# Optimization experiments

Measured on AMD Instinct MI355X. Metric: run time of the kernel, lower is better.

The kernel has to match this reference:

```python
import jax, jax.numpy as jnp
import numpy as np

B, L, D = 16384, 50, 32  # batch, history length, embedding_dim
NU, NI, NC = 100000, 100000, 1000


def setup_inputs() -> dict:
    key = jax.random.key(0)
    ks = jax.random.split(key, 16)
    customer_id = jax.random.randint(ks[0], (B,), 0, NU)
    candidate_good = jax.random.randint(ks[1], (B,), 0, NI)
    candidate_class = jax.random.randint(ks[2], (B,), 0, NC)
    history_goods = jax.random.randint(ks[3], (B, L), 0, NI)
    history_classes = jax.random.randint(ks[4], (B, L), 0, NC)
    user_table = jax.random.normal(ks[5], (NU, D), jnp.float32) * 0.05
    item_table = jax.random.normal(ks[6], (NI, D), jnp.float32) * 0.05
    item_table = item_table.at[0].set(0.0)  # padding_idx=0
    cat_table = jax.random.normal(ks[7], (NC, D), jnp.float32) * 0.05
    cat_table = cat_table.at[0].set(0.0)  # padding_idx=0
    # attention net: Linear(4*2D=256 -> 80), Linear(80 -> 1)
    aw1 = jax.random.normal(ks[8], (4 * 2 * D, 80), jnp.float32) * 0.05
    ab1 = jnp.zeros((80,), jnp.float32)
    aw2 = jax.random.normal(ks[9], (80, 1), jnp.float32) * 0.05
    ab2 = jnp.zeros((1,), jnp.float32)
    # final mlp: 5D=160 -> 256 -> 128 -> 1
    mw1 = jax.random.normal(ks[10], (5 * D, 256), jnp.float32) * 0.05
    mb1 = jnp.zeros((256,), jnp.float32)
    mw2 = jax.random.normal(ks[11], (256, 128), jnp.float32) * 0.05
    mb2 = jnp.zeros((128,), jnp.float32)
    mw3 = jax.random.normal(ks[12], (128, 1), jnp.float32) * 0.05
    mb3 = jnp.zeros((1,), jnp.float32)
    return dict(customer_id=customer_id, candidate_good=candidate_good,
                candidate_class=candidate_class, history_goods=history_goods,
                history_classes=history_classes, user_table=user_table,
                item_table=item_table, cat_table=cat_table,
                aw1=aw1, ab1=ab1, aw2=aw2, ab2=ab2,
                mw1=mw1, mb1=mb1, mw2=mw2, mb2=mb2, mw3=mw3, mb3=mb3)


def reference(customer_id, candidate_good, candidate_class, history_goods,
              history_classes, user_table, item_table, cat_table,
              aw1, ab1, aw2, ab2, mw1, mb1, mw2, mb2, mw3, mb3):
    user_emb = user_table[customer_id]                               # [B, D]
    cand = jnp.concatenate([item_table[candidate_good],
                            cat_table[candidate_class]], axis=-1)    # [B, 2D]
    hist = jnp.concatenate([item_table[history_goods],
                            cat_table[history_classes]], axis=-1)    # [B, L, 2D]
    q = jnp.broadcast_to(cand[:, None, :], hist.shape)               # [B, L, 2D]
    info = jnp.concatenate([q, hist, q - hist, q * hist], axis=-1)   # [B, L, 8D]
    h = jax.nn.relu(info @ aw1 + ab1)                                # [B, L, 80]
    scores = (h @ aw2 + ab2)[..., 0]                                 # [B, L]
    mask = history_goods != 0
    scores = jnp.where(mask, scores, -1e9)
    weights = jax.nn.softmax(scores, axis=1)                         # [B, L]
    att = jnp.einsum('bl,bld->bd', weights, hist)                    # [B, 2D]
    combined = jnp.concatenate([user_emb, cand, att], axis=-1)       # [B, 5D]
    z = jax.nn.relu(combined @ mw1 + mb1)
    z = jax.nn.relu(z @ mw2 + mb2)
    out = (z @ mw3 + mb3)[..., 0]                                    # [B]
    return out
```

## Files before the change

kernel.cpp:

```cpp
#include <hip/hip_runtime.h>
#include <math.h>

#define LHIST 50

typedef __attribute__((ext_vector_type(8))) short bf16x8;
typedef __attribute__((ext_vector_type(4))) float f32x4;

__device__ __forceinline__ unsigned short f2bf(float f) {
    union { float f; unsigned u; } v; v.f = f;
    unsigned r = v.u + 0x7fff + ((v.u >> 16) & 1);
    return (unsigned short)(r >> 16);
}
__device__ __forceinline__ float bf2f(unsigned short h) {
    union { unsigned u; float f; } v; v.u = ((unsigned)h) << 16;
    return v.f;
}
__device__ __forceinline__ unsigned packbf2(float lo, float hi) {
    return (unsigned)f2bf(lo) | ((unsigned)f2bf(hi) << 16);
}


__global__ void prep_kernel(const float* __restrict__ aw1,
                            const float* __restrict__ mw1,
                            const float* __restrict__ mw2,
                            const float* __restrict__ item_table,
                            const float* __restrict__ cat_table,
                            int itemN, int catN,
                            float* __restrict__ Awt,
                            unsigned short* __restrict__ Bmfb,
                            unsigned short* __restrict__ W4fb,
                            unsigned short* __restrict__ W1f,
                            unsigned short* __restrict__ W2f,
                            unsigned short* __restrict__ itemb,
                            unsigned short* __restrict__ catb) {
    int i = blockIdx.x * 256 + threadIdx.x;
    int i8 = i * 8;
    if (i8 + 7 < itemN) {
        float4 a = *(const float4*)&item_table[i8];
        float4 b = *(const float4*)&item_table[i8 + 4];
        uint4 r;
        r.x = packbf2(a.x, a.y); r.y = packbf2(a.z, a.w);
        r.z = packbf2(b.x, b.y); r.w = packbf2(b.z, b.w);
        *(uint4*)&itemb[i8] = r;
    }
    if (i8 + 7 < catN) {
        float4 a = *(const float4*)&cat_table[i8];
        float4 b = *(const float4*)&cat_table[i8 + 4];
        uint4 r;
        r.x = packbf2(a.x, a.y); r.y = packbf2(a.z, a.w);
        r.z = packbf2(b.x, b.y); r.w = packbf2(b.z, b.w);
        *(uint4*)&catb[i8] = r;
    }
    if (i < 5120) {
        int j = i >> 6, k = i & 63;
        Awt[i] = aw1[k * 80 + j] + aw1[(128 + k) * 80 + j];
        int kk = i / 80, n = i - kk * 80;
        int nt = n >> 4, colw = n & 15, ks = kk >> 5, r = kk & 31, qd = r >> 3, off = r & 7;
        int d = ((nt * 2 + ks) * 64 + qd * 16 + colw) * 8 + off;
        Bmfb[d] = f2bf(aw1[(64 + kk) * 80 + n] - aw1[(128 + kk) * 80 + n]);
        W4fb[d] = f2bf(aw1[(192 + kk) * 80 + n]);
    }
    if (i < 40960) {
        int kk = i >> 8, n = i & 255;
        int nt = n >> 4, colw = n & 15, ks = kk >> 5, r = kk & 31, qd = r >> 3, off = r & 7;
        W1f[((nt * 5 + ks) * 64 + qd * 16 + colw) * 8 + off] = f2bf(mw1[i]);
    }
    if (i < 32768) {
        int kk = i >> 7, n = i & 127;
        int nt = n >> 4, colw = n & 15, ks = kk >> 5, r = kk & 31, qd = r >> 3, off = r & 7;
        W2f[((nt * 8 + ks) * 64 + qd * 16 + colw) * 8 + off] = f2bf(mw2[i]);
    }
}

__global__ void __launch_bounds__(256, 4) attn_kernel(
    const int* __restrict__ cid, const int* __restrict__ cg,
    const int* __restrict__ cc,  const int* __restrict__ hg,
    const int* __restrict__ hc,
    const float* __restrict__ user_table, const float* __restrict__ item_table,
    const float* __restrict__ cat_table,
    const float* __restrict__ ab1, const float* __restrict__ aw2,
    const float* __restrict__ Awt, const unsigned short* __restrict__ Bmfb,
    const unsigned short* __restrict__ W4fb,
    const unsigned short* __restrict__ itemb, const unsigned short* __restrict__ catb,
    unsigned short* __restrict__ cfrag)
{
    __shared__ __align__(16) unsigned short sh_Bq[4][5120];
    __shared__ __align__(16) float sh_q[4][64];
    __shared__ float sh_bias[4][80];
    __shared__ float sh_sc[4][64];
    __shared__ float sh_aw2[80];
    __shared__ __align__(16) float sh_att[4][64];

    const int t = threadIdx.x;
    const int b0 = blockIdx.x * 4;
    const int wv = t >> 6;
    const int lane = t & 63;
    const int quad = lane >> 4;
    const int col = lane & 15;
    const int b = b0 + wv;

    int il[4], ic[4];
    #pragma unroll
    for (int mt = 0; mt < 4; ++mt) {
        int l = mt * 16 + col;
        int lc = (l < LHIST) ? l : 0;
        il[mt] = hg[b * LHIST + lc];
        ic[mt] = hc[b * LHIST + lc];
    }
    uint4 vi[4], vc[4];
    #pragma unroll
    for (int mt = 0; mt < 4; ++mt) {
        vi[mt] = *(const uint4*)&itemb[(size_t)il[mt] * 32 + quad * 8];
        vc[mt] = *(const uint4*)&catb[(size_t)ic[mt] * 32 + quad * 8];
    }
    {
        float v = (lane < 32) ? item_table[(size_t)cg[b] * 32 + lane]
                              : cat_table[(size_t)cc[b] * 32 + (lane - 32)];
        sh_q[wv][lane] = v;
    }
    if (t < 80) sh_aw2[t] = aw2[t];
    __syncthreads();

    #pragma unroll
    for (int it = 0; it < 10; ++it) {
        int i = it * 256 + t;
        int bb = i / 640;
        int j = (i - bb * 640) * 8;
        int lane8 = (j >> 3) & 63, ks = (j >> 9) & 1;
        int kk = ks * 32 + (lane8 >> 4) * 8;
        uint4 bm4 = *(const uint4*)&Bmfb[j];
        uint4 w44 = *(const uint4*)&W4fb[j];
        float4 qa = *(const float4*)&sh_q[bb][kk];
        float4 qb = *(const float4*)&sh_q[bb][kk + 4];
        unsigned bmw[4] = {bm4.x, bm4.y, bm4.z, bm4.w};
        unsigned w4w[4] = {w44.x, w44.y, w44.z, w44.w};
        float qv[8] = {qa.x, qa.y, qa.z, qa.w, qb.x, qb.y, qb.z, qb.w};
        uint4 res;
        unsigned* rp = (unsigned*)&res;
        #pragma unroll
        for (int d = 0; d < 4; ++d) {
            float lo = bf2f((unsigned short)(bmw[d] & 0xffff)) + qv[2 * d]     * bf2f((unsigned short)(w4w[d] & 0xffff));
            float hi = bf2f((unsigned short)(bmw[d] >> 16))    + qv[2 * d + 1] * bf2f((unsigned short)(w4w[d] >> 16));
            rp[d] = packbf2(lo, hi);
        }
        *(uint4*)&sh_Bq[bb][j] = res;
    }
    for (int s = t; s < 320; s += 256) {
        int bi = s / 80, j = s - bi * 80;
        float acc = ab1[j];
        const float4* aw = (const float4*)&Awt[j * 64];
        #pragma unroll
        for (int k4 = 0; k4 < 16; ++k4) {
            float4 a = aw[k4];
            float4 q = *(const float4*)&sh_q[bi][k4 * 4];
            acc += a.x * q.x + a.y * q.y + a.z * q.z + a.w * q.w;
        }
        sh_bias[bi][j] = acc;
    }
    __syncthreads();

    float bias_v[5], a2_v[5];
    #pragma unroll
    for (int nt = 0; nt < 5; ++nt) {
        bias_v[nt] = sh_bias[wv][nt * 16 + col];
        a2_v[nt]   = sh_aw2[nt * 16 + col];
    }

    #pragma unroll
    for (int p = 0; p < 2; ++p) {
        f32x4 acc[2][5];
        #pragma unroll
        for (int mi = 0; mi < 2; ++mi)
            #pragma unroll
            for (int nt = 0; nt < 5; ++nt) acc[mi][nt] = (f32x4){0.f,0.f,0.f,0.f};
        bf16x8 a0i = *(bf16x8*)&vi[p * 2];
        bf16x8 a0c = *(bf16x8*)&vc[p * 2];
        bf16x8 a1i = *(bf16x8*)&vi[p * 2 + 1];
        bf16x8 a1c = *(bf16x8*)&vc[p * 2 + 1];
        #pragma unroll
        for (int nt = 0; nt < 5; ++nt) {
            bf16x8 b0 = *(const bf16x8*)&sh_Bq[wv][((nt * 2 + 0) * 64 + lane) * 8];
            acc[0][nt] = __builtin_amdgcn_mfma_f32_16x16x32_bf16(a0i, b0, acc[0][nt], 0, 0, 0);
            acc[1][nt] = __builtin_amdgcn_mfma_f32_16x16x32_bf16(a1i, b0, acc[1][nt], 0, 0, 0);
            bf16x8 b1 = *(const bf16x8*)&sh_Bq[wv][((nt * 2 + 1) * 64 + lane) * 8];
            acc[0][nt] = __builtin_amdgcn_mfma_f32_16x16x32_bf16(a0c, b1, acc[0][nt], 0, 0, 0);
            acc[1][nt] = __builtin_amdgcn_mfma_f32_16x16x32_bf16(a1c, b1, acc[1][nt], 0, 0, 0);
        }
        #pragma unroll
        for (int mi = 0; mi < 2; ++mi) {
            int mt = p * 2 + mi;
            #pragma unroll
            for (int i = 0; i < 4; ++i) {
                float pp = 0.f;
                #pragma unroll
                for (int nt = 0; nt < 5; ++nt) {
                    float u = acc[mi][nt][i] + bias_v[nt];
                    pp += fmaxf(u, 0.f) * a2_v[nt];
                }
                pp += __shfl_xor(pp, 1);
                pp += __shfl_xor(pp, 2);
                pp += __shfl_xor(pp, 4);
                pp += __shfl_xor(pp, 8);
                if (col == 0) sh_sc[wv][mt * 16 + quad * 4 + i] = pp;
            }
        }
    }

    float sc = -INFINITY;
    if (lane < LHIST) {
        sc = sh_sc[wv][lane];
        if (hg[b * LHIST + lane] == 0) sc = -1e9f;
    }
    float m = sc;
    #pragma unroll
    for (int off = 32; off > 0; off >>= 1) m = fmaxf(m, __shfl_xor(m, off));
    float e = (lane < LHIST) ? __expf(sc - m) : 0.f;
    float ssum = e;
    #pragma unroll
    for (int off = 32; off > 0; off >>= 1) ssum += __shfl_xor(ssum, off);
    float w = e / ssum;

    {
        float wl[4];
        wl[0] = __shfl(w, col);
        wl[1] = __shfl(w, 16 + col);
        wl[2] = __shfl(w, 32 + col);
        wl[3] = __shfl(w, 48 + col);
        float at0[8], at1[8];
        #pragma unroll
        for (int j = 0; j < 8; ++j) { at0[j] = 0.f; at1[j] = 0.f; }
        #pragma unroll
        for (int mt = 0; mt < 4; ++mt) {
            union { uint4 u; unsigned short s[8]; } hi, hcv;
            hi.u = vi[mt]; hcv.u = vc[mt];
            #pragma unroll
            for (int j = 0; j < 8; ++j) {
                at0[j] += wl[mt] * bf2f(hi.s[j]);
                at1[j] += wl[mt] * bf2f(hcv.s[j]);
            }
        }
        #pragma unroll
        for (int off = 1; off < 16; off <<= 1)
            #pragma unroll
            for (int j = 0; j < 8; ++j) {
                at0[j] += __shfl_xor(at0[j], off);
                at1[j] += __shfl_xor(at1[j], off);
            }
        if (col == 0) {
            *(float4*)&sh_att[wv][quad * 8]     = make_float4(at0[0], at0[1], at0[2], at0[3]);
            *(float4*)&sh_att[wv][quad * 8 + 4] = make_float4(at0[4], at0[5], at0[6], at0[7]);
            *(float4*)&sh_att[wv][32 + quad * 8]     = make_float4(at1[0], at1[1], at1[2], at1[3]);
            *(float4*)&sh_att[wv][32 + quad * 8 + 4] = make_float4(at1[4], at1[5], at1[6], at1[7]);
        }
    }

    {
        int g = b >> 4, colm = b & 15;
        unsigned short* base = cfrag + (size_t)g * 2560;
        if (lane < 8) {
            float4 aa = *(const float4*)&sh_att[wv][lane * 8];
            float4 ab = *(const float4*)&sh_att[wv][lane * 8 + 4];
            int k0 = 96 + lane * 8;
            int ks = k0 >> 5, qd = (k0 >> 3) & 3;
            uint4 r;
            r.x = packbf2(aa.x, aa.y); r.y = packbf2(aa.z, aa.w);
            r.z = packbf2(ab.x, ab.y); r.w = packbf2(ab.z, ab.w);
            *(uint4*)(base + ((ks * 64) + qd * 16 + colm) * 8) = r;
        } else if (lane < 16) {
            int cq = lane - 8;
            int k0 = 32 + cq * 8;
            int ks = k0 >> 5, qd = (k0 >> 3) & 3;
            float4 qa = *(const float4*)&sh_q[wv][cq * 8];
            float4 qb = *(const float4*)&sh_q[wv][cq * 8 + 4];
            uint4 r;
            r.x = packbf2(qa.x, qa.y); r.y = packbf2(qa.z, qa.w);
            r.z = packbf2(qb.x, qb.y); r.w = packbf2(qb.z, qb.w);
            *(uint4*)(base + ((ks * 64) + qd * 16 + colm) * 8) = r;
        } else if (lane < 20) {
            int cu = lane - 16;
            int uidx = cid[b];
            float4 ua = *(const float4*)&user_table[(size_t)uidx * 32 + cu * 8];
            float4 ub = *(const float4*)&user_table[(size_t)uidx * 32 + cu * 8 + 4];
            uint4 r;
            r.x = packbf2(ua.x, ua.y); r.y = packbf2(ua.z, ua.w);
            r.z = packbf2(ub.x, ub.y); r.w = packbf2(ub.z, ub.w);
            *(uint4*)(base + (cu * 16 + colm) * 8) = r;
        }
    }
}

__global__ void __launch_bounds__(256, 4) mlp_kernel(
    const unsigned short* __restrict__ cfrag,
    const unsigned short* __restrict__ W1f, const unsigned short* __restrict__ W2f,
    const float* __restrict__ mb1, const float* __restrict__ mb2,
    const float* __restrict__ mw3, const float* __restrict__ mb3,
    float* __restrict__ out)
{
    __shared__ __align__(16) unsigned short shA2[4096];
    __shared__ float sh_part[4][16];

    const int t = threadIdx.x;
    const int g = blockIdx.x;
    const int wv = t >> 6;
    const int lane = t & 63;
    const int quad = lane >> 4;
    const int col = lane & 15;
    const unsigned short* abase = cfrag + (size_t)g * 2560;

    f32x4 acc1[4];
    #pragma unroll
    for (int j = 0; j < 4; ++j) acc1[j] = (f32x4){0.f, 0.f, 0.f, 0.f};
    #pragma unroll
    for (int ks = 0; ks < 5; ++ks) {
        bf16x8 a = *(const bf16x8*)&abase[(ks * 64 + lane) * 8];
        #pragma unroll
        for (int j = 0; j < 4; ++j) {
            bf16x8 bw = *(const bf16x8*)&W1f[(((wv * 4 + j) * 5 + ks) * 64 + lane) * 8];
            acc1[j] = __builtin_amdgcn_mfma_f32_16x16x32_bf16(a, bw, acc1[j], 0, 0, 0);
        }
    }
    #pragma unroll
    for (int j = 0; j < 4; ++j) {
        int n = (wv * 4 + j) * 16 + col;
        float bj = mb1[n];
        int ks2 = n >> 5, qd2 = (n >> 3) & 3, off2 = n & 7;
        #pragma unroll
        for (int i = 0; i < 4; ++i) {
            float z = fmaxf(acc1[j][i] + bj, 0.f);
            shA2[(ks2 * 64 + qd2 * 16 + quad * 4 + i) * 8 + off2] = f2bf(z);
        }
    }
    __syncthreads();

    f32x4 acc2[2];
    #pragma unroll
    for (int jj = 0; jj < 2; ++jj) acc2[jj] = (f32x4){0.f, 0.f, 0.f, 0.f};
    #pragma unroll
    for (int ks = 0; ks < 8; ++ks) {
        bf16x8 a = *(const bf16x8*)&shA2[(ks * 64 + lane) * 8];
        #pragma unroll
        for (int jj = 0; jj < 2; ++jj) {
            bf16x8 bw = *(const bf16x8*)&W2f[(((wv * 2 + jj) * 8 + ks) * 64 + lane) * 8];
            acc2[jj] = __builtin_amdgcn_mfma_f32_16x16x32_bf16(a, bw, acc2[jj], 0, 0, 0);
        }
    }
    #pragma unroll
    for (int i = 0; i < 4; ++i) {
        float p = 0.f;
        #pragma unroll
        for (int jj = 0; jj < 2; ++jj) {
            int n = (wv * 2 + jj) * 16 + col;
            float z = fmaxf(acc2[jj][i] + mb2[n], 0.f);
            p += z * mw3[n];
        }
        p += __shfl_xor(p, 1);
        p += __shfl_xor(p, 2);
        p += __shfl_xor(p, 4);
        p += __shfl_xor(p, 8);
        if (col == 0) sh_part[wv][quad * 4 + i] = p;
    }
    __syncthreads();
    if (t < 16)
        out[g * 16 + t] = sh_part[0][t] + sh_part[1][t] + sh_part[2][t] + sh_part[3][t] + mb3[0];
}

extern "C" void kernel_launch(void* const* d_in, const int* in_sizes, int n_in,
                              void* d_out, int out_size, void* d_ws, size_t ws_size,
                              hipStream_t stream) {
    const int*   cid = (const int*)d_in[0];
    const int*   cg  = (const int*)d_in[1];
    const int*   cc  = (const int*)d_in[2];
    const int*   hg  = (const int*)d_in[3];
    const int*   hc  = (const int*)d_in[4];
    const float* user_table = (const float*)d_in[5];
    const float* item_table = (const float*)d_in[6];
    const float* cat_table  = (const float*)d_in[7];
    const float* aw1 = (const float*)d_in[8];
    const float* ab1 = (const float*)d_in[9];
    const float* aw2 = (const float*)d_in[10];
    const float* mw1 = (const float*)d_in[12];
    const float* mb1 = (const float*)d_in[13];
    const float* mw2 = (const float*)d_in[14];
    const float* mb2 = (const float*)d_in[15];
    const float* mw3 = (const float*)d_in[16];
    const float* mb3 = (const float*)d_in[17];
    float* out = (float*)d_out;

    const int B = in_sizes[0];
    const int itemN = in_sizes[6];
    const int catN  = in_sizes[7];
    float* ws = (float*)d_ws;
    float* Awt = ws;
    unsigned short* Bmfb = (unsigned short*)(ws + 5120);
    unsigned short* W4fb = (unsigned short*)(ws + 7680);
    unsigned short* W1f  = (unsigned short*)(ws + 10240);
    unsigned short* W2f  = (unsigned short*)(ws + 30720);
    unsigned short* itemb = (unsigned short*)(ws + 47104);
    unsigned short* catb  = itemb + itemN;
    unsigned short* cfrag = (unsigned short*)(ws + 47104 + (itemN + catN + 1) / 2);

    int n8 = (itemN + 7) / 8;
    int prep_grid = (n8 + 255) / 256;
    if (prep_grid < 160) prep_grid = 160;
    prep_kernel<<<prep_grid, 256, 0, stream>>>(aw1, mw1, mw2, item_table, cat_table,
                                               itemN, catN, Awt, Bmfb, W4fb, W1f, W2f,
                                               itemb, catb);
    attn_kernel<<<B / 4, 256, 0, stream>>>(cid, cg, cc, hg, hc,
                                           user_table, item_table, cat_table,
                                           ab1, aw2, Awt, Bmfb, W4fb, itemb, catb, cfrag);
    mlp_kernel<<<B / 16, 256, 0, stream>>>(cfrag, W1f, W2f,
                                           mb1, mb2, mw3, mb3, out);
}
```

Measured before the change: 211.5 us.

## Split each attention row across two waves and shrink attn blocks to two rows

The attention kernel now handles two batch rows per 256-thread block, with two waves sharing each row's 50-step history (32 positions each). Partial attention sums from the two halves are combined through shared memory before writing the MLP input fragment. This halves per-block shared memory and per-wave registers, doubles the grid, and raises the launch-bounds occupancy target to improve latency hiding on the gather-heavy kernel. It adds extra block barriers and a cross-wave reduction. Separately, bf16 packing switches to the HIP intrinsic conversion.

```diff
diff --git a/kernel.cpp b/kernel.cpp
--- a/kernel.cpp
+++ b/kernel.cpp
@@ -1,4 +1,5 @@
 #include <hip/hip_runtime.h>
+#include <hip/hip_bf16.h>
 #include <math.h>
 
 #define LHIST 50
@@ -18,6 +19,12 @@
 __device__ __forceinline__ unsigned packbf2(float lo, float hi) {
     return (unsigned)f2bf(lo) | ((unsigned)f2bf(hi) << 16);
 }
+__device__ __forceinline__ unsigned pk2(float lo, float hi) {
+    __hip_bfloat162 h = __float22bfloat162_rn(make_float2(lo, hi));
+    return *(unsigned*)&h;
+}
+__device__ __forceinline__ float bflo(unsigned u){ union{unsigned v;float f;} x; x.v = u << 16; return x.f; }
+__device__ __forceinline__ float bfhi(unsigned u){ union{unsigned v;float f;} x; x.v = u & 0xffff0000u; return x.f; }
 
 
 __global__ void prep_kernel(const float* __restrict__ aw1,
@@ -39,16 +46,16 @@
         float4 a = *(const float4*)&item_table[i8];
         float4 b = *(const float4*)&item_table[i8 + 4];
         uint4 r;
-        r.x = packbf2(a.x, a.y); r.y = packbf2(a.z, a.w);
-        r.z = packbf2(b.x, b.y); r.w = packbf2(b.z, b.w);
+        r.x = pk2(a.x, a.y); r.y = pk2(a.z, a.w);
+        r.z = pk2(b.x, b.y); r.w = pk2(b.z, b.w);
         *(uint4*)&itemb[i8] = r;
     }
     if (i8 + 7 < catN) {
         float4 a = *(const float4*)&cat_table[i8];
         float4 b = *(const float4*)&cat_table[i8 + 4];
         uint4 r;
-        r.x = packbf2(a.x, a.y); r.y = packbf2(a.z, a.w);
-        r.z = packbf2(b.x, b.y); r.w = packbf2(b.z, b.w);
+        r.x = pk2(a.x, a.y); r.y = pk2(a.z, a.w);
+        r.z = pk2(b.x, b.y); r.w = pk2(b.z, b.w);
         *(uint4*)&catb[i8] = r;
     }
     if (i < 5120) {
@@ -72,7 +79,7 @@
     }
 }
 
-__global__ void __launch_bounds__(256, 4) attn_kernel(
+__global__ void __launch_bounds__(256, 6) attn_kernel(
     const int* __restrict__ cid, const int* __restrict__ cg,
     const int* __restrict__ cc,  const int* __restrict__ hg,
     const int* __restrict__ hc,
@@ -84,69 +91,78 @@
     const unsigned short* __restrict__ itemb, const unsigned short* __restrict__ catb,
     unsigned short* __restrict__ cfrag)
 {
-    __shared__ __align__(16) unsigned short sh_Bq[4][5120];
-    __shared__ __align__(16) float sh_q[4][64];
-    __shared__ float sh_bias[4][80];
-    __shared__ float sh_sc[4][64];
+    __shared__ __align__(16) unsigned short sh_Bq[2][5120];
+    __shared__ __align__(16) float sh_q[2][64];
+    __shared__ float sh_bias[2][80];
+    __shared__ float sh_sc[2][64];
     __shared__ float sh_aw2[80];
-    __shared__ __align__(16) float sh_att[4][64];
+    __shared__ __align__(16) float sh_att[2][2][64];
 
     const int t = threadIdx.x;
-    const int b0 = blockIdx.x * 4;
+    const int b0 = blockIdx.x * 2;
     const int wv = t >> 6;
     const int lane = t & 63;
     const int quad = lane >> 4;
     const int col = lane & 15;
-    const int b = b0 + wv;
-
-    int il[4], ic[4];
-    #pragma unroll
-    for (int mt = 0; mt < 4; ++mt) {
-        int l = mt * 16 + col;
+    const int bb = wv >> 1;
+    const int hwv = wv & 1;
+    const int b = b0 + bb;
+
+    int il[2], ic[2];
+    #pragma unroll
+    for (int mi = 0; mi < 2; ++mi) {
+        int l = hwv * 32 + mi * 16 + col;
         int lc = (l < LHIST) ? l : 0;
-        il[mt] = hg[b * LHIST + lc];
-        ic[mt] = hc[b * LHIST + lc];
-    }
-    uint4 vi[4], vc[4];
-    #pragma unroll
-    for (int mt = 0; mt < 4; ++mt) {
-        vi[mt] = *(const uint4*)&itemb[(size_t)il[mt] * 32 + quad * 8];
-        vc[mt] = *(const uint4*)&catb[(size_t)ic[mt] * 32 + quad * 8];
-    }
-    {
-        float v = (lane < 32) ? item_table[(size_t)cg[b] * 32 + lane]
-                              : cat_table[(size_t)cc[b] * 32 + (lane - 32)];
-        sh_q[wv][lane] = v;
+        il[mi] = hg[b * LHIST + lc];
+        ic[mi] = hc[b * LHIST + lc];
+    }
+    uint4 vi[2], vc[2];
+    #pragma unroll
+    for (int mi = 0; mi < 2; ++mi) {
+        vi[mi] = *(const uint4*)&itemb[(size_t)il[mi] * 32 + quad * 8];
+        vc[mi] = *(const uint4*)&catb[(size_t)ic[mi] * 32 + quad * 8];
+    }
+    if (t < 128) {
+        int qbi = t >> 6, k = t & 63;
+        int bq = b0 + qbi;
+        float v = (k < 32) ? item_table[(size_t)cg[bq] * 32 + k]
+                           : cat_table[(size_t)cc[bq] * 32 + (k - 32)];
+        sh_q[qbi][k] = v;
     }
     if (t < 80) sh_aw2[t] = aw2[t];
     __syncthreads();
 
-    #pragma unroll
-    for (int it = 0; it < 10; ++it) {
-        int i = it * 256 + t;
-        int bb = i / 640;
-        int j = (i - bb * 640) * 8;
-        int lane8 = (j >> 3) & 63, ks = (j >> 9) & 1;
+    for (int slot = t; slot < 640; slot += 256) {
+        int j = slot * 8;
+        int lane8 = slot & 63, ks = (slot >> 6) & 1;
         int kk = ks * 32 + (lane8 >> 4) * 8;
         uint4 bm4 = *(const uint4*)&Bmfb[j];
         uint4 w44 = *(const uint4*)&W4fb[j];
-        float4 qa = *(const float4*)&sh_q[bb][kk];
-        float4 qb = *(const float4*)&sh_q[bb][kk + 4];
-        unsigned bmw[4] = {bm4.x, bm4.y, bm4.z, bm4.w};
-        unsigned w4w[4] = {w44.x, w44.y, w44.z, w44.w};
-        float qv[8] = {qa.x, qa.y, qa.z, qa.w, qb.x, qb.y, qb.z, qb.w};
-        uint4 res;
-        unsigned* rp = (unsigned*)&res;
+        unsigned bw[4] = {bm4.x, bm4.y, bm4.z, bm4.w};
+        unsigned ww[4] = {w44.x, w44.y, w44.z, w44.w};
+        float bl[8], wl4[8];
         #pragma unroll
         for (int d = 0; d < 4; ++d) {
-            float lo = bf2f((unsigned short)(bmw[d] & 0xffff)) + qv[2 * d]     * bf2f((unsigned short)(w4w[d] & 0xffff));
-            float hi = bf2f((unsigned short)(bmw[d] >> 16))    + qv[2 * d + 1] * bf2f((unsigned short)(w4w[d] >> 16));
-            rp[d] = packbf2(lo, hi);
-        }
-        *(uint4*)&sh_Bq[bb][j] = res;
-    }
-    for (int s = t; s < 320; s += 256) {
-        int bi = s / 80, j = s - bi * 80;
+            bl[2 * d] = bflo(bw[d]);  bl[2 * d + 1] = bfhi(bw[d]);
+            wl4[2 * d] = bflo(ww[d]); wl4[2 * d + 1] = bfhi(ww[d]);
+        }
+        #pragma unroll
+        for (int bb2 = 0; bb2 < 2; ++bb2) {
+            float4 qa = *(const float4*)&sh_q[bb2][kk];
+            float4 qb = *(const float4*)&sh_q[bb2][kk + 4];
+            float qv[8] = {qa.x, qa.y, qa.z, qa.w, qb.x, qb.y, qb.z, qb.w};
+            uint4 res;
+            unsigned* rp = (unsigned*)&res;
+            #pragma unroll
+            for (int d = 0; d < 4; ++d)
+                rp[d] = pk2(bl[2 * d]     + qv[2 * d]     * wl4[2 * d],
+                            bl[2 * d + 1] + qv[2 * d + 1] * wl4[2 * d + 1]);
+            *(uint4*)&sh_Bq[bb2][j] = res;
+        }
+    }
+    if (t < 160) {
+        int bi = t >= 80;
+        int j = t - bi * 80;
         float acc = ab1[j];
         const float4* aw = (const float4*)&Awt[j * 64];
         #pragma unroll
@@ -162,53 +178,50 @@
     float bias_v[5], a2_v[5];
     #pragma unroll
     for (int nt = 0; nt < 5; ++nt) {
-        bias_v[nt] = sh_bias[wv][nt * 16 + col];
+        bias_v[nt] = sh_bias[bb][nt * 16 + col];
         a2_v[nt]   = sh_aw2[nt * 16 + col];
     }
-
-    #pragma unroll
-    for (int p = 0; p < 2; ++p) {
-        f32x4 acc[2][5];
-        #pragma unroll
-        for (int mi = 0; mi < 2; ++mi)
+    f32x4 acc[2][5];
+    #pragma unroll
+    for (int mi = 0; mi < 2; ++mi)
+        #pragma unroll
+        for (int nt = 0; nt < 5; ++nt) acc[mi][nt] = (f32x4){0.f, 0.f, 0.f, 0.f};
+    bf16x8 a0i = *(bf16x8*)&vi[0];
+    bf16x8 a0c = *(bf16x8*)&vc[0];
+    bf16x8 a1i = *(bf16x8*)&vi[1];
+    bf16x8 a1c = *(bf16x8*)&vc[1];
+    #pragma unroll
+    for (int nt = 0; nt < 5; ++nt) {
+        bf16x8 bfr0 = *(const bf16x8*)&sh_Bq[bb][((nt * 2 + 0) * 64 + lane) * 8];
+        acc[0][nt] = __builtin_amdgcn_mfma_f32_16x16x32_bf16(a0i, bfr0, acc[0][nt], 0, 0, 0);
+        acc[1][nt] = __builtin_amdgcn_mfma_f32_16x16x32_bf16(a1i, bfr0, acc[1][nt], 0, 0, 0);
+        bf16x8 bfr1 = *(const bf16x8*)&sh_Bq[bb][((nt * 2 + 1) * 64 + lane) * 8];
+        acc[0][nt] = __builtin_amdgcn_mfma_f32_16x16x32_bf16(a0c, bfr1, acc[0][nt], 0, 0, 0);
+        acc[1][nt] = __builtin_amdgcn_mfma_f32_16x16x32_bf16(a1c, bfr1, acc[1][nt], 0, 0, 0);
+    }
+    #pragma unroll
+    for (int mi = 0; mi < 2; ++mi) {
+        int lbase = hwv * 32 + mi * 16 + quad * 4;
+        #pragma unroll
+        for (int i = 0; i < 4; ++i) {
+            float pp = 0.f;
             #pragma unroll
-            for (int nt = 0; nt < 5; ++nt) acc[mi][nt] = (f32x4){0.f,0.f,0.f,0.f};
-        bf16x8 a0i = *(bf16x8*)&vi[p * 2];
-        bf16x8 a0c = *(bf16x8*)&vc[p * 2];
-        bf16x8 a1i = *(bf16x8*)&vi[p * 2 + 1];
-        bf16x8 a1c = *(bf16x8*)&vc[p * 2 + 1];
-        #pragma unroll
-        for (int nt = 0; nt < 5; ++nt) {
-            bf16x8 b0 = *(const bf16x8*)&sh_Bq[wv][((nt * 2 + 0) * 64 + lane) * 8];
-            acc[0][nt] = __builtin_amdgcn_mfma_f32_16x16x32_bf16(a0i, b0, acc[0][nt], 0, 0, 0);
-            acc[1][nt] = __builtin_amdgcn_mfma_f32_16x16x32_bf16(a1i, b0, acc[1][nt], 0, 0, 0);
-            bf16x8 b1 = *(const bf16x8*)&sh_Bq[wv][((nt * 2 + 1) * 64 + lane) * 8];
-            acc[0][nt] = __builtin_amdgcn_mfma_f32_16x16x32_bf16(a0c, b1, acc[0][nt], 0, 0, 0);
-            acc[1][nt] = __builtin_amdgcn_mfma_f32_16x16x32_bf16(a1c, b1, acc[1][nt], 0, 0, 0);
-        }
-        #pragma unroll
-        for (int mi = 0; mi < 2; ++mi) {
-            int mt = p * 2 + mi;
-            #pragma unroll
-            for (int i = 0; i < 4; ++i) {
-                float pp = 0.f;
-                #pragma unroll
-                for (int nt = 0; nt < 5; ++nt) {
-                    float u = acc[mi][nt][i] + bias_v[nt];
-                    pp += fmaxf(u, 0.f) * a2_v[nt];
-                }
-                pp += __shfl_xor(pp, 1);
-                pp += __shfl_xor(pp, 2);
-                pp += __shfl_xor(pp, 4);
-                pp += __shfl_xor(pp, 8);
-                if (col == 0) sh_sc[wv][mt * 16 + quad * 4 + i] = pp;
+            for (int nt = 0; nt < 5; ++nt) {
+                float u = acc[mi][nt][i] + bias_v[nt];
+                pp += fmaxf(u, 0.f) * a2_v[nt];
             }
-        }
-    }
+            pp += __shfl_xor(pp, 1);
+            pp += __shfl_xor(pp, 2);
+            pp += __shfl_xor(pp, 4);
+            pp += __shfl_xor(pp, 8);
+            if (col == 0) sh_sc[bb][lbase + i] = pp;
+        }
+    }
+    __syncthreads();
 
     float sc = -INFINITY;
     if (lane < LHIST) {
-        sc = sh_sc[wv][lane];
+        sc = sh_sc[bb][lane];
         if (hg[b * LHIST + lane] == 0) sc = -1e9f;
     }
     float m = sc;
@@ -221,22 +234,20 @@
     float w = e / ssum;
 
     {
-        float wl[4];
-        wl[0] = __shfl(w, col);
-        wl[1] = __shfl(w, 16 + col);
-        wl[2] = __shfl(w, 32 + col);
-        wl[3] = __shfl(w, 48 + col);
+        float wl[2];
+        wl[0] = __shfl(w, hwv * 32 + col);
+        wl[1] = __shfl(w, hwv * 32 + 16 + col);
         float at0[8], at1[8];
         #pragma unroll
         for (int j = 0; j < 8; ++j) { at0[j] = 0.f; at1[j] = 0.f; }
         #pragma unroll
-        for (int mt = 0; mt < 4; ++mt) {
+        for (int mi = 0; mi < 2; ++mi) {
             union { uint4 u; unsigned short s[8]; } hi, hcv;
-            hi.u = vi[mt]; hcv.u = vc[mt];
+            hi.u = vi[mi]; hcv.u = vc[mi];
             #pragma unroll
             for (int j = 0; j < 8; ++j) {
-                at0[j] += wl[mt] * bf2f(hi.s[j]);
-                at1[j] += wl[mt] * bf2f(hcv.s[j]);
+                at0[j] += wl[mi] * bf2f(hi.s[j]);
+                at1[j] += wl[mi] * bf2f(hcv.s[j]);
             }
         }
         #pragma unroll
@@ -247,24 +258,28 @@
                 at1[j] += __shfl_xor(at1[j], off);
             }
         if (col == 0) {
-            *(float4*)&sh_att[wv][quad * 8]     = make_float4(at0[0], at0[1], at0[2], at0[3]);
-            *(float4*)&sh_att[wv][quad * 8 + 4] = make_float4(at0[4], at0[5], at0[6], at0[7]);
-            *(float4*)&sh_att[wv][32 + quad * 8]     = make_float4(at1[0], at1[1], at1[2], at1[3]);
-            *(float4*)&sh_att[wv][32 + quad * 8 + 4] = make_float4(at1[4], at1[5], at1[6], at1[7]);
-        }
-    }
-
-    {
-        int g = b >> 4, colm = b & 15;
+            *(float4*)&sh_att[bb][hwv][quad * 8]     = make_float4(at0[0], at0[1], at0[2], at0[3]);
+            *(float4*)&sh_att[bb][hwv][quad * 8 + 4] = make_float4(at0[4], at0[5], at0[6], at0[7]);
+            *(float4*)&sh_att[bb][hwv][32 + quad * 8]     = make_float4(at1[0], at1[1], at1[2], at1[3]);
+            *(float4*)&sh_att[bb][hwv][32 + quad * 8 + 4] = make_float4(at1[4], at1[5], at1[6], at1[7]);
+        }
+    }
+    __syncthreads();
+
+    if (wv < 2) {
+        int bo = b0 + wv;
+        int g = bo >> 4, colm = bo & 15;
         unsigned short* base = cfrag + (size_t)g * 2560;
         if (lane < 8) {
-            float4 aa = *(const float4*)&sh_att[wv][lane * 8];
-            float4 ab = *(const float4*)&sh_att[wv][lane * 8 + 4];
+            float4 a0 = *(const float4*)&sh_att[wv][0][lane * 8];
+            float4 a1 = *(const float4*)&sh_att[wv][1][lane * 8];
+            float4 b0v = *(const float4*)&sh_att[wv][0][lane * 8 + 4];
+            float4 b1v = *(const float4*)&sh_att[wv][1][lane * 8 + 4];
             int k0 = 96 + lane * 8;
             int ks = k0 >> 5, qd = (k0 >> 3) & 3;
             uint4 r;
-            r.x = packbf2(aa.x, aa.y); r.y = packbf2(aa.z, aa.w);
-            r.z = packbf2(ab.x, ab.y); r.w = packbf2(ab.z, ab.w);
+            r.x = pk2(a0.x + a1.x, a0.y + a1.y); r.y = pk2(a0.z + a1.z, a0.w + a1.w);
+            r.z = pk2(b0v.x + b1v.x, b0v.y + b1v.y); r.w = pk2(b0v.z + b1v.z, b0v.w + b1v.w);
             *(uint4*)(base + ((ks * 64) + qd * 16 + colm) * 8) = r;
         } else if (lane < 16) {
             int cq = lane - 8;
@@ -273,17 +288,17 @@
             float4 qa = *(const float4*)&sh_q[wv][cq * 8];
             float4 qb = *(const float4*)&sh_q[wv][cq * 8 + 4];
             uint4 r;
-            r.x = packbf2(qa.x, qa.y); r.y = packbf2(qa.z, qa.w);
-            r.z = packbf2(qb.x, qb.y); r.w = packbf2(qb.z, qb.w);
+            r.x = pk2(qa.x, qa.y); r.y = pk2(qa.z, qa.w);
+            r.z = pk2(qb.x, qb.y); r.w = pk2(qb.z, qb.w);
             *(uint4*)(base + ((ks * 64) + qd * 16 + colm) * 8) = r;
         } else if (lane < 20) {
             int cu = lane - 16;
-            int uidx = cid[b];
+            int uidx = cid[bo];
             float4 ua = *(const float4*)&user_table[(size_t)uidx * 32 + cu * 8];
             float4 ub = *(const float4*)&user_table[(size_t)uidx * 32 + cu * 8 + 4];
             uint4 r;
-            r.x = packbf2(ua.x, ua.y); r.y = packbf2(ua.z, ua.w);
-            r.z = packbf2(ub.x, ub.y); r.w = packbf2(ub.z, ub.w);
+            r.x = pk2(ua.x, ua.y); r.y = pk2(ua.z, ua.w);
+            r.z = pk2(ub.x, ub.y); r.w = pk2(ub.z, ub.w);
             *(uint4*)(base + (cu * 16 + colm) * 8) = r;
         }
     }
@@ -405,7 +420,7 @@
     prep_kernel<<<prep_grid, 256, 0, stream>>>(aw1, mw1, mw2, item_table, cat_table,
                                                itemN, catN, Awt, Bmfb, W4fb, W1f, W2f,
                                                itemb, catb);
-    attn_kernel<<<B / 4, 256, 0, stream>>>(cid, cg, cc, hg, hc,
+    attn_kernel<<<B / 2, 256, 0, stream>>>(cid, cg, cc, hg, hc,
                                            user_table, item_table, cat_table,
                                            ab1, aw2, Awt, Bmfb, W4fb, itemb, catb, cfrag);
     mlp_kernel<<<B / 16, 256, 0, stream>>>(cfrag, W1f, W2f,
```

New measurement: 202.4 us. 1.04x faster.
